# Kernel optimization log

Measured on AMD Instinct MI355X. Metric: run time of the kernel, lower is better.

## Reference

```python
import jax, jax.numpy as jnp
import numpy as np

KERNEL = 5
STRIDE = 1
D = 32
B = 8
L = 2048


def setup_inputs() -> dict:
    key = jax.random.key(0)
    k1, k2, k3, k4, k5 = jax.random.split(key, 5)
    dd = D * D
    scale_dense = 1.0 / np.sqrt(dd)
    scale_attn = 1.0 / np.sqrt(dd * KERNEL)
    return {
        "inputs": jax.random.normal(k1, (B, L, D, D), dtype=jnp.float32),
        "W_dense": jax.random.normal(k2, (dd, dd), dtype=jnp.float32) * scale_dense,
        "b_dense": jax.random.normal(k3, (dd,), dtype=jnp.float32) * scale_dense,
        "W_attn": jax.random.normal(k4, (KERNEL, dd * KERNEL), dtype=jnp.float32) * scale_attn,
        "b_attn": jax.random.normal(k5, (KERNEL,), dtype=jnp.float32) * scale_attn,
    }


def _forward(inputs, W_dense, b_dense, W_attn, b_attn):
    b, l, d, _ = inputs.shape
    pad = KERNEL - 1
    pad_left, pad_right = pad // 2, (pad - 1) // 2 + 1

    # Linear2D: linear over flattened d*d dims
    h = jnp.einsum('blde,fe->bldf',
                   inputs.reshape(b, l, d * d)[..., None, :].squeeze(-2).reshape(b, l, 1, d * d),
                   W_dense).reshape(b, l, d * d) + b_dense
    h = h.reshape(b, l, d, d)

    # pad_identity: pad seq dim with identity matrices (neutral for matrix chain)
    eye = jnp.broadcast_to(jnp.eye(d, dtype=inputs.dtype), (b, 1, d, d))
    h_pad = jnp.concatenate(
        [jnp.broadcast_to(eye, (b, pad_left, d, d)), h,
         jnp.broadcast_to(eye, (b, pad_right, d, d))], axis=1)

    out_len = (l + pad - KERNEL) // STRIDE + 1
    # unfold(dim=1, size=KERNEL, step=STRIDE) -> [b, out_len, d, d, KERNEL]
    h_unf = jnp.stack([h_pad[:, k * 1: k + out_len * STRIDE: STRIDE][:, :out_len]
                       for k in range(KERNEL)], axis=-1)

    attention_inputs = h_unf.reshape(b, out_len, d * d * KERNEL)
    scores = attention_inputs @ W_attn.T + b_attn          # [b, out_len, KERNEL]
    alpha = jax.nn.softmax(jax.nn.leaky_relu(scores, 0.01), axis=2)
    alpha = alpha.reshape(b, out_len, 1, 1, KERNEL)

    h_attn = alpha * h_unf                                  # [b, out_len, d, d, KERNEL]
    out = h_attn[..., 0]
    for i in range(1, KERNEL):
        out = jnp.einsum('bcij,bcjk->bcik', out, h_attn[..., i])
    return out


def reference(inputs, W_dense, b_dense, W_attn, b_attn):
    return _forward(inputs, W_dense, b_dense, W_attn, b_attn)
```

## Files before the change

### kernel.cpp

```cpp
#include <hip/hip_runtime.h>
#include <stdint.h>

typedef float  f32x4  __attribute__((ext_vector_type(4)));
typedef float  f32x16 __attribute__((ext_vector_type(16)));
typedef short  s16x8  __attribute__((ext_vector_type(8)));
typedef unsigned short u16x4 __attribute__((ext_vector_type(4)));

#define LPAD 2052

__device__ __forceinline__ float bf2f(unsigned short u){
  unsigned v = ((unsigned)u) << 16;
  return __builtin_bit_cast(float, v);
}
__device__ __forceinline__ unsigned short f2bf(float f){
  unsigned u = __builtin_bit_cast(unsigned, f);
  u += 0x7fffu + ((u >> 16) & 1u);
  return (unsigned short)(u >> 16);
}
__device__ __forceinline__ unsigned cvt_pk_bf16(float lo, float hi){
  unsigned r;
  asm volatile("v_cvt_pk_bf16_f32 %0, %1, %2" : "=v"(r) : "v"(lo), "v"(hi));
  return r;
}

__global__ void k_cvtx(const float* __restrict__ src, unsigned short* __restrict__ dst){
  int b = blockIdx.x;
  int bb = (b & 7) * 2048 + (b >> 3);
  int i = bb * 256 + threadIdx.x;
  f32x4 v = ((const f32x4*)src)[i];
  u16x4 o;
  o[0] = f2bf(v[0]); o[1] = f2bf(v[1]); o[2] = f2bf(v[2]); o[3] = f2bf(v[3]);
  ((u16x4*)dst)[i] = o;
}

__global__ void k_cvt(const float* __restrict__ src, unsigned short* __restrict__ dst, int n4){
  int i = blockIdx.x * 256 + threadIdx.x;
  if (i >= n4) return;
  f32x4 v = ((const f32x4*)src)[i];
  u16x4 o;
  o[0] = f2bf(v[0]); o[1] = f2bf(v[1]); o[2] = f2bf(v[2]); o[3] = f2bf(v[3]);
  ((u16x4*)dst)[i] = o;
}

__global__ void k_eye(unsigned short* __restrict__ H){
  int t = blockIdx.x * 256 + threadIdx.x;
  int b = t >> 12;
  int r = t & 4095;
  int which = r >> 10;
  int ij = r & 1023;
  int p = (which < 2) ? which : (2048 + which);
  H[((size_t)(b * LPAD + p) << 10) + ij] = ((ij >> 5) == (ij & 31)) ? 0x3F80 : 0;
}

__global__ void k_wprep(const float* __restrict__ Wa, unsigned short* __restrict__ Wa2g){
  int t = blockIdx.x * 256 + threadIdx.x;
  int col = t >> 10, e = t & 1023;
  int f = col / 5, kk = col - 5 * f;
  unsigned short v = 0;
  if (col < 25) v = f2bf(Wa[f * 5120 + e * 5 + kk]);
  Wa2g[t] = v;
}

#define MFMA16 __builtin_amdgcn_mfma_f32_16x16x32_bf16

__global__ __launch_bounds__(512, 4) void k_gemm2(const unsigned short* __restrict__ A,
                                                  const unsigned short* __restrict__ Bw,
                                                  const float* __restrict__ bias,
                                                  unsigned short* __restrict__ H){
  __shared__ __align__(128) unsigned short lds[24576];
  const int tid = threadIdx.x;
  const int wid = tid >> 6, l = tid & 63;
  const int wm = wid >> 1, wn = wid & 1;
  const int lm = l & 15, lk = l >> 4;
  const int hb = blockIdx.x;
  const int xcd = hb & 7, sl = hb >> 3;
  const int bm = xcd * 8 + (sl >> 3), bn = sl & 7;
  const int M0 = bm * 256, N0 = bn * 128;

  const unsigned ko0 = (unsigned)((lk ^ (lm & 7)) << 4);
  const unsigned ko1 = ko0 ^ 64u;
  const unsigned rA = ((unsigned)(wm * 64 + lm)) * 128u;
  const unsigned rB = 32768u + ((unsigned)(wn * 64 + lm)) * 128u;

  f32x4 acc[4][4] = {};

  for (int kt = 0; kt < 16; ++kt){
    const int ktK = kt * 64;
    #pragma unroll
    for (int j = 0; j < 6; j++){
      unsigned d = (unsigned)(j * 512 + tid) * 16;
      const unsigned short* g;
      if (j < 4){
        unsigned row = d >> 7;
        unsigned srcC = ((d >> 4) & 7u) ^ (row & 7u);
        g = A + (size_t)(M0 + row) * 1024 + ktK + srcC * 8;
      } else {
        unsigned db = d - 32768u;
        unsigned row = db >> 7;
        unsigned srcC = ((db >> 4) & 7u) ^ (row & 7u);
        g = Bw + (size_t)(N0 + row) * 1024 + ktK + srcC * 8;
      }
      __builtin_amdgcn_global_load_lds((const __attribute__((address_space(1))) void*)g,
                                       (__attribute__((address_space(3))) void*)&lds[d >> 1],
                                       16, 0, 0);
    }
    __syncthreads();

    s16x8 a0[4], b0[4];
    #pragma unroll
    for (int m = 0; m < 4; m++) a0[m] = *(const s16x8*)&lds[(rA + m * 2048u + ko0) >> 1];
    #pragma unroll
    for (int n = 0; n < 4; n++) b0[n] = *(const s16x8*)&lds[(rB + n * 2048u + ko0) >> 1];
    #pragma unroll
    for (int m = 0; m < 4; m++){
      #pragma unroll
      for (int n = 0; n < 4; n++)
        acc[m][n] = MFMA16(a0[m], b0[n], acc[m][n], 0, 0, 0);
    }
    #pragma unroll
    for (int m = 0; m < 4; m++) a0[m] = *(const s16x8*)&lds[(rA + m * 2048u + ko1) >> 1];
    #pragma unroll
    for (int n = 0; n < 4; n++) b0[n] = *(const s16x8*)&lds[(rB + n * 2048u + ko1) >> 1];
    #pragma unroll
    for (int m = 0; m < 4; m++){
      #pragma unroll
      for (int n = 0; n < 4; n++)
        acc[m][n] = MFMA16(a0[m], b0[n], acc[m][n], 0, 0, 0);
    }
    __syncthreads();
  }

  float bv[4];
  #pragma unroll
  for (int n = 0; n < 4; n++) bv[n] = bias[N0 + wn * 64 + n * 16 + lm];
  #pragma unroll
  for (int m = 0; m < 4; m++){
    #pragma unroll
    for (int r = 0; r < 4; r++){
      int gm = M0 + wm * 64 + m * 16 + lk * 4 + r;
      int bb = gm >> 11, li = gm & 2047;
      unsigned short* orow = H + ((size_t)(bb * LPAD + 2 + li) << 10);
      #pragma unroll
      for (int n = 0; n < 4; n++){
        orow[N0 + wn * 64 + n * 16 + lm] = f2bf(acc[m][n][r] + bv[n]);
      }
    }
  }
}

__global__ __launch_bounds__(256) void k_part(const unsigned short* __restrict__ H,
                                              const unsigned short* __restrict__ Wa2g,
                                              float* __restrict__ part){
  __shared__ unsigned short sB[32768];
  const int tid = threadIdx.x;
  const int wv = tid >> 6, l = tid & 63;
  const int lm = l & 15, lk = l >> 4;
  #pragma unroll
  for (int j = 0; j < 16; j++){
    unsigned d = (unsigned)(j * 256 + tid) * 16;
    unsigned col = d >> 11;
    unsigned srcC = ((d >> 4) & 127u) ^ (col & 7u);
    const unsigned short* g = Wa2g + col * 1024 + srcC * 8;
    __builtin_amdgcn_global_load_lds((const __attribute__((address_space(1))) void*)g,
                                     (__attribute__((address_space(3))) void*)&sB[d >> 1],
                                     16, 0, 0);
  }
  __syncthreads();
  const int rbase = blockIdx.x * 128 + wv * 32;
  f32x4 acc[2][2] = {};
  for (int kk = 0; kk < 1024; kk += 32){
    s16x8 aF[2], bF[2];
    #pragma unroll
    for (int m = 0; m < 2; m++)
      aF[m] = *(const s16x8*)(H + (size_t)(rbase + m * 16 + lm) * 1024 + kk + lk * 8);
    #pragma unroll
    for (int n = 0; n < 2; n++){
      unsigned col = (unsigned)(n * 16 + lm);
      unsigned c = (unsigned)(kk >> 3) + (unsigned)lk;
      bF[n] = *(const s16x8*)&sB[(col * 2048u + ((c ^ (col & 7u)) << 4)) >> 1];
    }
    #pragma unroll
    for (int m = 0; m < 2; m++){
      #pragma unroll
      for (int n = 0; n < 2; n++)
        acc[m][n] = MFMA16(aF[m], bF[n], acc[m][n], 0, 0, 0);
    }
  }
  #pragma unroll
  for (int m = 0; m < 2; m++){
    #pragma unroll
    for (int r = 0; r < 4; r++){
      int row = rbase + m * 16 + lk * 4 + r;
      #pragma unroll
      for (int n = 0; n < 2; n++)
        part[(size_t)row * 32 + n * 16 + lm] = acc[m][n][r];
    }
  }
}

__global__ __launch_bounds__(256) void k_chain(const unsigned short* __restrict__ H,
                                               const float* __restrict__ part,
                                               const float* __restrict__ battn,
                                               float* __restrict__ out){
  const int tid = threadIdx.x;
  const int w = tid >> 6, l = tid & 63;
  const int blk = (blockIdx.x & 7) * 512 + (blockIdx.x >> 3);
  const int pos = blk * 4 + w;
  const int bb = pos >> 11, li = pos & 2047;
  const unsigned short* hbase = H + ((size_t)(bb * LPAD + li) << 10);
  const int col = l & 31;
  const int kh = (l >> 5) << 3;

  const float* prow = part + (size_t)(bb * LPAD + li) * 32;
  float sc[5];
  #pragma unroll
  for (int f = 0; f < 5; f++){
    float a = battn[f];
    #pragma unroll
    for (int k = 0; k < 5; k++)
      a += prow[k * 32 + f * 5 + k];
    sc[f] = (a > 0.f) ? a : 0.01f * a;
  }
  float mx = sc[0];
  #pragma unroll
  for (int f = 1; f < 5; f++) mx = fmaxf(mx, sc[f]);
  float e0 = expf(sc[0] - mx), e1 = expf(sc[1] - mx), e2 = expf(sc[2] - mx),
        e3 = expf(sc[3] - mx), e4 = expf(sc[4] - mx);
  float ssum = e0 + e1 + e2 + e3 + e4;
  float inv = 1.f / ssum;
  float inv2 = inv * inv;
  const float sv = (e0 * e1 * e2 * e3 * e4) * inv2 * inv2 * inv;

  const unsigned short* h4 = hbase + 4 * 1024;
  unsigned q0, q1, q2, q3, q4, q5, q6, q7;
  {
    #define LD2(kk) ((unsigned)h4[(kk) * 32 + col] | ((unsigned)h4[((kk) + 1) * 32 + col] << 16))
    q0 = LD2(kh + 0);  q1 = LD2(kh + 2);  q2 = LD2(kh + 4);  q3 = LD2(kh + 6);
    q4 = LD2(kh + 16); q5 = LD2(kh + 18); q6 = LD2(kh + 20); q7 = LD2(kh + 22);
    #undef LD2
  }
  union { unsigned u[4]; s16x8 v; } ub0, ub1;
  ub0.u[0] = q0; ub0.u[1] = q1; ub0.u[2] = q2; ub0.u[3] = q3;
  ub1.u[0] = q4; ub1.u[1] = q5; ub1.u[2] = q6; ub1.u[3] = q7;
  s16x8 Bf0 = ub0.v, Bf1 = ub1.v;

  f32x16 acc;
  #pragma unroll
  for (int st = 0; st < 4; st++){
    const int km = 3 - st;
    const unsigned short* hA = hbase + (km << 10);
    s16x8 A0 = *(const s16x8*)(hA + col * 32 + kh);
    s16x8 A1 = *(const s16x8*)(hA + col * 32 + kh + 16);
    f32x16 z = {0,0,0,0,0,0,0,0,0,0,0,0,0,0,0,0};
    acc = __builtin_amdgcn_mfma_f32_32x32x16_bf16(A0, Bf0, z,   0, 0, 0);
    acc = __builtin_amdgcn_mfma_f32_32x32x16_bf16(A1, Bf1, acc, 0, 0, 0);
    if (st < 3){
      unsigned d0 = cvt_pk_bf16(acc[0],  acc[1]);
      unsigned d1 = cvt_pk_bf16(acc[2],  acc[3]);
      unsigned d2 = cvt_pk_bf16(acc[4],  acc[5]);
      unsigned d3 = cvt_pk_bf16(acc[6],  acc[7]);
      unsigned d4 = cvt_pk_bf16(acc[8],  acc[9]);
      unsigned d5 = cvt_pk_bf16(acc[10], acc[11]);
      unsigned d6 = cvt_pk_bf16(acc[12], acc[13]);
      unsigned d7 = cvt_pk_bf16(acc[14], acc[15]);
      unsigned p0 = __shfl_xor(d0, 32, 64);
      unsigned p1 = __shfl_xor(d1, 32, 64);
      unsigned p2 = __shfl_xor(d2, 32, 64);
      unsigned p3 = __shfl_xor(d3, 32, 64);
      unsigned p4 = __shfl_xor(d4, 32, 64);
      unsigned p5 = __shfl_xor(d5, 32, 64);
      unsigned p6 = __shfl_xor(d6, 32, 64);
      unsigned p7 = __shfl_xor(d7, 32, 64);
      const bool lo = (l < 32);
      ub0.u[0] = lo ? d0 : p2;  ub0.u[1] = lo ? d1 : p3;
      ub0.u[2] = lo ? p0 : d2;  ub0.u[3] = lo ? p1 : d3;
      ub1.u[0] = lo ? d4 : p6;  ub1.u[1] = lo ? d5 : p7;
      ub1.u[2] = lo ? p4 : d6;  ub1.u[3] = lo ? p5 : d7;
      Bf0 = ub0.v; Bf1 = ub1.v;
    }
  }

  float* ob = out + ((size_t)pos << 10);
  #pragma unroll
  for (int t = 0; t < 16; t++){
    int row = (t & 3) + 8 * (t >> 2) + ((l >> 5) << 2);
    ob[row * 32 + col] = sv * acc[t];
  }
}

extern "C" void kernel_launch(void* const* d_in, const int* in_sizes, int n_in,
                              void* d_out, int out_size, void* d_ws, size_t ws_size,
                              hipStream_t stream){
  const float* X  = (const float*)d_in[0];
  const float* Wd = (const float*)d_in[1];
  const float* bd = (const float*)d_in[2];
  const float* Wa = (const float*)d_in[3];
  const float* ba = (const float*)d_in[4];
  float* out = (float*)d_out;

  char* ws = (char*)d_ws;
  unsigned short* Hpad = (unsigned short*)ws;
  unsigned short* Wbf  = (unsigned short*)(ws + 33619968);
  unsigned short* Wa2g = (unsigned short*)(ws + 33619968 + 2097152);
  float*          part = (float*)(ws + 33619968 + 2097152 + 65536);
  unsigned short* Xbf  = (unsigned short*)d_out;

  k_cvtx<<<16384, 256, 0, stream>>>(X, Xbf);
  k_cvt<<<1024, 256, 0, stream>>>(Wd, Wbf, 262144);
  k_eye<<<128, 256, 0, stream>>>(Hpad);
  k_wprep<<<128, 256, 0, stream>>>(Wa, Wa2g);
  k_gemm2<<<512, 512, 0, stream>>>(Xbf, Wbf, bd, Hpad);
  k_part<<<129, 256, 0, stream>>>(Hpad, Wa2g, part);
  k_chain<<<4096, 256, 0, stream>>>(Hpad, part, ba, out);
}
```

Before: 94.53 us.

## Fuse fp32-to-bf16 input conversion into GEMM and merge prep kernels

Drops the separate pass that converted the 64MB fp32 input to bf16. The GEMM now loads fp32 X tiles straight into LDS and converts them to bf16 in registers with v_cvt_pk_bf16 before the MFMA. The three small prep kernels (weight cast, identity padding, attention weight prep) are merged into one launch. This removes a full read plus write of the converted input and several launches, but doubles the A-tile LDS footprint to 80KB, which may lower GEMM occupancy and adds conversion ALU work inside the inner loop.

```diff
diff --git a/kernel.cpp b/kernel.cpp
--- a/kernel.cpp
+++ b/kernel.cpp
@@ -23,51 +23,41 @@
   return r;
 }
 
-__global__ void k_cvtx(const float* __restrict__ src, unsigned short* __restrict__ dst){
-  int b = blockIdx.x;
-  int bb = (b & 7) * 2048 + (b >> 3);
-  int i = bb * 256 + threadIdx.x;
-  f32x4 v = ((const f32x4*)src)[i];
-  u16x4 o;
-  o[0] = f2bf(v[0]); o[1] = f2bf(v[1]); o[2] = f2bf(v[2]); o[3] = f2bf(v[3]);
-  ((u16x4*)dst)[i] = o;
-}
-
-__global__ void k_cvt(const float* __restrict__ src, unsigned short* __restrict__ dst, int n4){
-  int i = blockIdx.x * 256 + threadIdx.x;
-  if (i >= n4) return;
-  f32x4 v = ((const f32x4*)src)[i];
-  u16x4 o;
-  o[0] = f2bf(v[0]); o[1] = f2bf(v[1]); o[2] = f2bf(v[2]); o[3] = f2bf(v[3]);
-  ((u16x4*)dst)[i] = o;
-}
-
-__global__ void k_eye(unsigned short* __restrict__ H){
-  int t = blockIdx.x * 256 + threadIdx.x;
-  int b = t >> 12;
-  int r = t & 4095;
-  int which = r >> 10;
-  int ij = r & 1023;
-  int p = (which < 2) ? which : (2048 + which);
-  H[((size_t)(b * LPAD + p) << 10) + ij] = ((ij >> 5) == (ij & 31)) ? 0x3F80 : 0;
-}
-
-__global__ void k_wprep(const float* __restrict__ Wa, unsigned short* __restrict__ Wa2g){
-  int t = blockIdx.x * 256 + threadIdx.x;
-  int col = t >> 10, e = t & 1023;
-  int f = col / 5, kk = col - 5 * f;
-  unsigned short v = 0;
-  if (col < 25) v = f2bf(Wa[f * 5120 + e * 5 + kk]);
-  Wa2g[t] = v;
+__global__ void k_prep(const float* __restrict__ Wd, unsigned short* __restrict__ Wbf,
+                       unsigned short* __restrict__ H,
+                       const float* __restrict__ Wa, unsigned short* __restrict__ Wa2g){
+  const int b = blockIdx.x;
+  if (b < 1024){
+    int i = b * 256 + threadIdx.x;
+    f32x4 v = ((const f32x4*)Wd)[i];
+    u16x4 o;
+    o[0] = f2bf(v[0]); o[1] = f2bf(v[1]); o[2] = f2bf(v[2]); o[3] = f2bf(v[3]);
+    ((u16x4*)Wbf)[i] = o;
+  } else if (b < 1152){
+    int t = (b - 1024) * 256 + threadIdx.x;
+    int bt = t >> 12;
+    int r = t & 4095;
+    int which = r >> 10;
+    int ij = r & 1023;
+    int p = (which < 2) ? which : (2048 + which);
+    H[((size_t)(bt * LPAD + p) << 10) + ij] = ((ij >> 5) == (ij & 31)) ? 0x3F80 : 0;
+  } else {
+    int t = (b - 1152) * 256 + threadIdx.x;
+    int col = t >> 10, e = t & 1023;
+    int f = col / 5, kk = col - 5 * f;
+    unsigned short v = 0;
+    if (col < 25) v = f2bf(Wa[f * 5120 + e * 5 + kk]);
+    Wa2g[t] = v;
+  }
 }
 
 #define MFMA16 __builtin_amdgcn_mfma_f32_16x16x32_bf16
 
-__global__ __launch_bounds__(512, 4) void k_gemm2(const unsigned short* __restrict__ A,
-                                                  const unsigned short* __restrict__ Bw,
-                                                  const float* __restrict__ bias,
-                                                  unsigned short* __restrict__ H){
-  __shared__ __align__(128) unsigned short lds[24576];
+__global__ __launch_bounds__(512, 4) void k_gemm2f(const float* __restrict__ X,
+                                                   const unsigned short* __restrict__ Bw,
+                                                   const float* __restrict__ bias,
+                                                   unsigned short* __restrict__ H){
+  __shared__ __align__(128) unsigned short lds[40960];
   const int tid = threadIdx.x;
   const int wid = tid >> 6, l = tid & 63;
   const int wm = wid >> 1, wn = wid & 1;
@@ -77,55 +67,62 @@
   const int bm = xcd * 8 + (sl >> 3), bn = sl & 7;
   const int M0 = bm * 256, N0 = bn * 128;
 
-  const unsigned ko0 = (unsigned)((lk ^ (lm & 7)) << 4);
-  const unsigned ko1 = ko0 ^ 64u;
-  const unsigned rA = ((unsigned)(wm * 64 + lm)) * 128u;
-  const unsigned rB = 32768u + ((unsigned)(wn * 64 + lm)) * 128u;
+  const unsigned koB0 = (unsigned)((lk ^ (lm & 7)) << 4);
+  const unsigned koB1 = koB0 ^ 64u;
+  const unsigned rBb = 65536u + ((unsigned)(wn * 64 + lm)) * 128u;
 
   f32x4 acc[4][4] = {};
 
   for (int kt = 0; kt < 16; ++kt){
     const int ktK = kt * 64;
     #pragma unroll
-    for (int j = 0; j < 6; j++){
+    for (int j = 0; j < 8; j++){
       unsigned d = (unsigned)(j * 512 + tid) * 16;
-      const unsigned short* g;
-      if (j < 4){
-        unsigned row = d >> 7;
-        unsigned srcC = ((d >> 4) & 7u) ^ (row & 7u);
-        g = A + (size_t)(M0 + row) * 1024 + ktK + srcC * 8;
-      } else {
-        unsigned db = d - 32768u;
-        unsigned row = db >> 7;
-        unsigned srcC = ((db >> 4) & 7u) ^ (row & 7u);
-        g = Bw + (size_t)(N0 + row) * 1024 + ktK + srcC * 8;
-      }
+      unsigned row = d >> 8;
+      unsigned cs = ((d >> 4) & 15u) ^ (row & 7u);
+      const float* g = X + (size_t)(M0 + row) * 1024 + ktK + cs * 4u;
       __builtin_amdgcn_global_load_lds((const __attribute__((address_space(1))) void*)g,
                                        (__attribute__((address_space(3))) void*)&lds[d >> 1],
                                        16, 0, 0);
     }
+    #pragma unroll
+    for (int j = 0; j < 2; j++){
+      unsigned db = (unsigned)(j * 512 + tid) * 16;
+      unsigned row = db >> 7;
+      unsigned cs = ((db >> 4) & 7u) ^ (row & 7u);
+      const unsigned short* g = Bw + (size_t)(N0 + row) * 1024 + ktK + cs * 8u;
+      __builtin_amdgcn_global_load_lds((const __attribute__((address_space(1))) void*)g,
+                                       (__attribute__((address_space(3))) void*)&lds[(65536u + db) >> 1],
+                                       16, 0, 0);
+    }
     __syncthreads();
 
-    s16x8 a0[4], b0[4];
-    #pragma unroll
-    for (int m = 0; m < 4; m++) a0[m] = *(const s16x8*)&lds[(rA + m * 2048u + ko0) >> 1];
-    #pragma unroll
-    for (int n = 0; n < 4; n++) b0[n] = *(const s16x8*)&lds[(rB + n * 2048u + ko0) >> 1];
+    s16x8 b0[4], b1[4];
+    #pragma unroll
+    for (int n = 0; n < 4; n++){
+      b0[n] = *(const s16x8*)&lds[(rBb + n * 2048u + koB0) >> 1];
+      b1[n] = *(const s16x8*)&lds[(rBb + n * 2048u + koB1) >> 1];
+    }
     #pragma unroll
     for (int m = 0; m < 4; m++){
+      unsigned rr = (unsigned)(wm * 64 + m * 16 + lm);
+      unsigned base = rr * 256u;
+      unsigned r7 = rr & 7u;
       #pragma unroll
-      for (int n = 0; n < 4; n++)
-        acc[m][n] = MFMA16(a0[m], b0[n], acc[m][n], 0, 0, 0);
-    }
-    #pragma unroll
-    for (int m = 0; m < 4; m++) a0[m] = *(const s16x8*)&lds[(rA + m * 2048u + ko1) >> 1];
-    #pragma unroll
-    for (int n = 0; n < 4; n++) b0[n] = *(const s16x8*)&lds[(rB + n * 2048u + ko1) >> 1];
-    #pragma unroll
-    for (int m = 0; m < 4; m++){
-      #pragma unroll
-      for (int n = 0; n < 4; n++)
-        acc[m][n] = MFMA16(a0[m], b0[n], acc[m][n], 0, 0, 0);
+      for (int h = 0; h < 2; h++){
+        unsigned c0 = ((unsigned)(h * 8 + 2 * lk))     ^ r7;
+        unsigned c1 = ((unsigned)(h * 8 + 2 * lk + 1)) ^ r7;
+        f32x4 lo = *(const f32x4*)&lds[(base + c0 * 16u) >> 1];
+        f32x4 hi = *(const f32x4*)&lds[(base + c1 * 16u) >> 1];
+        union { unsigned u[4]; s16x8 v; } af;
+        af.u[0] = cvt_pk_bf16(lo[0], lo[1]);
+        af.u[1] = cvt_pk_bf16(lo[2], lo[3]);
+        af.u[2] = cvt_pk_bf16(hi[0], hi[1]);
+        af.u[3] = cvt_pk_bf16(hi[2], hi[3]);
+        #pragma unroll
+        for (int n = 0; n < 4; n++)
+          acc[m][n] = MFMA16(af.v, (h == 0) ? b0[n] : b1[n], acc[m][n], 0, 0, 0);
+      }
     }
     __syncthreads();
   }
@@ -303,13 +300,9 @@
   unsigned short* Wbf  = (unsigned short*)(ws + 33619968);
   unsigned short* Wa2g = (unsigned short*)(ws + 33619968 + 2097152);
   float*          part = (float*)(ws + 33619968 + 2097152 + 65536);
-  unsigned short* Xbf  = (unsigned short*)d_out;
-
-  k_cvtx<<<16384, 256, 0, stream>>>(X, Xbf);
-  k_cvt<<<1024, 256, 0, stream>>>(Wd, Wbf, 262144);
-  k_eye<<<128, 256, 0, stream>>>(Hpad);
-  k_wprep<<<128, 256, 0, stream>>>(Wa, Wa2g);
-  k_gemm2<<<512, 512, 0, stream>>>(Xbf, Wbf, bd, Hpad);
+
+  k_prep<<<1280, 256, 0, stream>>>(Wd, Wbf, Hpad, Wa, Wa2g);
+  k_gemm2f<<<512, 512, 0, stream>>>(X, Wbf, bd, Hpad);
   k_part<<<129, 256, 0, stream>>>(Hpad, Wa2g, part);
   k_chain<<<4096, 256, 0, stream>>>(Hpad, part, ba, out);
 }
```

After: 104.1 us. 1.1x slower.
